# Kernel tuning notes

Hardware: AMD Instinct MI355X
Metric: run time of the kernel (lower is better)

The kernel has to match this reference:

```python
import jax, jax.numpy as jnp
import numpy as np

B, N, C = 32, 2048, 64  # graphs, points per graph, hidden channels


def _linear_params(key, fin, fout):
    k1, k2 = jax.random.split(key)
    bound = 1.0 / np.sqrt(fin)
    W = jax.random.uniform(k1, (fin, fout), minval=-bound, maxval=bound, dtype=jnp.float32)
    b = jax.random.uniform(k2, (fout,), minval=-bound, maxval=bound, dtype=jnp.float32)
    return W, b


def setup_inputs() -> dict:
    key = jax.random.key(0)
    ks = jax.random.split(key, 10)
    W1a, b1a = _linear_params(ks[0], 3 * 2 + 3, C)   # conv1 mlp layer 1 (h is pos, 3-dim)
    W1b, b1b = _linear_params(ks[1], C, C)
    W2a, b2a = _linear_params(ks[2], C * 2 + 3, C)   # conv2
    W2b, b2b = _linear_params(ks[3], C, C)
    W3a, b3a = _linear_params(ks[4], C * 2 + 3, C)   # conv3
    W3b, b3b = _linear_params(ks[5], C, C)
    Wr, br = _linear_params(ks[6], C, 6)
    pos = jax.random.normal(ks[7], (B * N, 3), dtype=jnp.float32)
    x = jax.random.normal(ks[8], (B * N, 3), dtype=jnp.float32)  # unused by forward (h=pos)
    batch = jnp.repeat(jnp.arange(B, dtype=jnp.int32), N)
    return dict(x=x, pos=pos, batch=batch,
                W1a=W1a, b1a=b1a, W1b=W1b, b1b=b1b,
                W2a=W2a, b2a=b2a, W2b=W2b, b2b=b2b,
                W3a=W3a, b3a=b3a, W3b=W3b, b3b=b3b,
                Wr=Wr, br=br)


_gather = jax.vmap(lambda a, i: a[i])  # per-graph fancy gather


def knn_idx(pos, k):
    # pos: [B, n, 3] -> idx [B, n, k] of k nearest neighbors (incl. self, loop=True)
    d2 = jnp.sum((pos[:, :, None, :] - pos[:, None, :, :]) ** 2, axis=-1)  # [B,n,n]
    _, idx = jax.lax.top_k(-d2, k)
    return idx


def fps_idx(pos_b, m):
    # farthest point sampling of m points from pos_b [n,3], deterministic start at 0
    d = jnp.sum((pos_b - pos_b[0]) ** 2, axis=-1)
    def body(d, _):
        i = jnp.argmax(d)
        d = jnp.minimum(d, jnp.sum((pos_b - pos_b[i]) ** 2, axis=-1))
        return d, i
    _, rest = jax.lax.scan(body, d, None, length=m - 1)
    return jnp.concatenate([jnp.zeros((1,), rest.dtype), rest])


def pointnet_layer(h, pos, idx, W1, b1, W2, b2):
    # h [B,n,Ch], pos [B,n,3], idx [B,n,k]; message = mlp(cat(h_i,h_j,pos_j-pos_i)); aggr = max
    h_j = _gather(h, idx)                      # [B,n,k,Ch]
    pos_j = _gather(pos, idx)                  # [B,n,k,3]
    rel = pos_j - pos[:, :, None, :]
    h_i = jnp.broadcast_to(h[:, :, None, :], h_j.shape)
    m = jnp.concatenate([h_i, h_j, rel], axis=-1)
    m = jax.nn.relu(m @ W1 + b1) @ W2 + b2
    return jnp.max(m, axis=2)                  # max over neighbors -> [B,n,C]


def reference(x, pos, batch,
              W1a, b1a, W1b, b1b,
              W2a, b2a, W2b, b2b,
              W3a, b3a, W3b, b3b,
              Wr, br):
    p = pos.reshape(B, N, 3)
    # layer 1: h = pos, k = 6
    h = jax.nn.relu(pointnet_layer(p, p, knn_idx(p, 6), W1a, b1a, W1b, b1b))
    # fps ratio 0.5 -> N/2
    sel = jax.vmap(lambda pb: fps_idx(pb, N // 2))(p)
    p, h = _gather(p, sel), _gather(h, sel)
    # layer 2: k = 4
    h = jax.nn.relu(pointnet_layer(h, p, knn_idx(p, 4), W2a, b2a, W2b, b2b))
    # fps -> N/4
    sel = jax.vmap(lambda pb: fps_idx(pb, N // 4))(p)
    p, h = _gather(p, sel), _gather(h, sel)
    # layer 3: k = 3
    h = jax.nn.relu(pointnet_layer(h, p, knn_idx(p, 3), W3a, b3a, W3b, b3b))
    g = jnp.max(h, axis=1)  # global max pool over points -> [B, C]
    return g @ Wr + br      # [B, 6]
```

## Files before the change

### kernel.cpp

```cpp
#include <hip/hip_runtime.h>
#include <hip/hip_bf16.h>
#include <math.h>

constexpr int B = 32;
constexpr int N = 2048;

__global__ void detect_kernel(const unsigned int* __restrict__ raw, int* __restrict__ flag) {
    __shared__ int cnt;
    if (threadIdx.x == 0) cnt = 0;
    __syncthreads();
    int c = 0;
    for (int i = threadIdx.x; i < 4096; i += 256) {
        unsigned h = (raw[i] >> 8) & 0x7f;
        if (h >= 0x3a && h <= 0x41) c++;
    }
    atomicAdd(&cnt, c);
    __syncthreads();
    if (threadIdx.x == 0) *flag = (cnt > (4096 * 55) / 100) ? 1 : 0;
}

__global__ void b2f_kernel(const void* __restrict__ in, float* __restrict__ out, int n,
                           const int* __restrict__ flag) {
    int i = blockIdx.x * 256 + threadIdx.x;
    if (i >= n) return;
    if (*flag) out[i] = __bfloat162float(((const __hip_bfloat16*)in)[i]);
    else       out[i] = ((const float*)in)[i];
}

struct B2FMulti {
    const void* src[14];
    float* dst[14];
    int n[14];
};

__global__ void b2f_multi_kernel(B2FMulti p, const int* __restrict__ flag) {
    int a = blockIdx.y;
    int i = blockIdx.x * 256 + threadIdx.x;
    if (i >= p.n[a]) return;
    if (*flag) p.dst[a][i] = __bfloat162float(((const __hip_bfloat16*)p.src[a])[i]);
    else       p.dst[a][i] = ((const float*)p.src[a])[i];
}

template <int K>
__global__ void __launch_bounds__(256) knn_kernel(const float* __restrict__ pos,
                                                  int* __restrict__ idx_out, int n) {
    #pragma clang fp contract(off)
    const int b = blockIdx.y;
    const int i = blockIdx.x * 256 + threadIdx.x;
    const float* pb = pos + (size_t)b * n * 3;
    const float xi = pb[i * 3 + 0], yi = pb[i * 3 + 1], zi = pb[i * 3 + 2];

    float bd[K];
    int   bi_[K];
    #pragma unroll
    for (int q = 0; q < K; ++q) { bd[q] = __builtin_inff(); bi_[q] = 0x7fffffff; }

    __shared__ float tx[256], ty[256], tz[256];
    for (int t0 = 0; t0 < n; t0 += 256) {
        __syncthreads();
        {
            int j = t0 + threadIdx.x;
            tx[threadIdx.x] = pb[j * 3 + 0];
            ty[threadIdx.x] = pb[j * 3 + 1];
            tz[threadIdx.x] = pb[j * 3 + 2];
        }
        __syncthreads();
        for (int jj = 0; jj < 256; ++jj) {
            float dx = xi - tx[jj], dy = yi - ty[jj], dz = zi - tz[jj];
            float d2 = (dx * dx + dy * dy) + dz * dz;
            int jg = t0 + jj;
            if (d2 < bd[K - 1] || (d2 == bd[K - 1] && jg < bi_[K - 1])) {
                bd[K - 1] = d2; bi_[K - 1] = jg;
                #pragma unroll
                for (int q = K - 1; q > 0; --q) {
                    bool sw = (bd[q] < bd[q - 1]) || (bd[q] == bd[q - 1] && bi_[q] < bi_[q - 1]);
                    if (sw) {
                        float td = bd[q]; bd[q] = bd[q - 1]; bd[q - 1] = td;
                        int   ti = bi_[q]; bi_[q] = bi_[q - 1]; bi_[q - 1] = ti;
                    }
                }
            }
        }
    }
    int* op = idx_out + ((size_t)b * n + i) * K;
    #pragma unroll
    for (int q = 0; q < K; ++q) op[q] = bi_[q];
}

template <int NPTS>
__device__ __forceinline__ void fps_phase(const float* __restrict__ px,
                                          const float* __restrict__ py,
                                          const float* __restrict__ pz,
                                          int* __restrict__ sel_lds,
                                          unsigned long long* __restrict__ slots,
                                          int m, int t) {
    #pragma clang fp contract(off)
    constexpr int P = NPTS / 256;
    float d[P], ox[P], oy[P], oz[P];
    unsigned int nk[P];
    const float sx = px[0], sy = py[0], sz = pz[0];
    #pragma unroll
    for (int p = 0; p < P; ++p) {
        const int ii = t * P + p;
        ox[p] = px[ii]; oy[p] = py[ii]; oz[p] = pz[ii];
        float dx = ox[p] - sx, dy = oy[p] - sy, dz = oz[p] - sz;
        d[p] = (dx * dx + dy * dy) + dz * dz;
        nk[p] = ~(unsigned)ii;
    }
    if (t == 0) sel_lds[0] = 0;

    for (int it = 1; it < m; ++it) {
        unsigned long long kb = ((unsigned long long)__float_as_uint(d[0]) << 32) | nk[0];
        #pragma unroll
        for (int p = 1; p < P; ++p) {
            unsigned long long key = ((unsigned long long)__float_as_uint(d[p]) << 32) | nk[p];
            if (key > kb) kb = key;
        }
        #pragma unroll
        for (int o = 1; o < 64; o <<= 1) {
            unsigned long long other = __shfl_xor(kb, o, 64);
            if (other > kb) kb = other;
        }
        if ((t & 63) == 0) slots[(it & 1) * 4 + (t >> 6)] = kb;
        __syncthreads();
        {
            const unsigned long long* sp = slots + (it & 1) * 4;
            unsigned long long k0 = sp[0], k1 = sp[1], k2 = sp[2], k3 = sp[3];
            if (k1 > k0) k0 = k1;
            if (k3 > k2) k2 = k3;
            kb = (k2 > k0) ? k2 : k0;
        }
        const int bix = (int)(~(unsigned)(kb & 0xffffffffULL));
        if (t == 0) sel_lds[it] = bix;
        const float nx = px[bix], ny = py[bix], nz = pz[bix];
        #pragma unroll
        for (int p = 0; p < P; ++p) {
            float dx = ox[p] - nx, dy = oy[p] - ny, dz = oz[p] - nz;
            float dd = (dx * dx + dy * dy) + dz * dz;
            d[p] = fminf(d[p], dd);
        }
    }
    __syncthreads();
}

__global__ void __launch_bounds__(256) mega_kernel(
        const float* __restrict__ posf, const int* __restrict__ idx1,
        const float* __restrict__ W1, const float* __restrict__ b1,
        const float* __restrict__ W2, const float* __restrict__ b2,
        float* __restrict__ h1, int* __restrict__ sel1, int* __restrict__ sel2,
        float* __restrict__ p2, float* __restrict__ p3) {
    __shared__ __align__(16) char smem[65536];
    const int t = threadIdx.x;

    if (blockIdx.x < B) {
        const int b = blockIdx.x;
        float* px = (float*)smem;
        float* py = px + 2048;
        float* pz = py + 2048;
        int*   sel1_l = (int*)(pz + 2048);
        float* qx = (float*)(sel1_l + 1024);
        float* qy = qx + 1024;
        float* qz = qy + 1024;
        int*   sel2_l = (int*)(qz + 1024);
        unsigned long long* slots = (unsigned long long*)(sel2_l + 512);

        const float* pb = posf + (size_t)b * N * 3;
        for (int i = t; i < N; i += 256) {
            px[i] = pb[i * 3 + 0]; py[i] = pb[i * 3 + 1]; pz[i] = pb[i * 3 + 2];
        }
        __syncthreads();

        fps_phase<2048>(px, py, pz, sel1_l, slots, 1024, t);

        for (int i = t; i < 1024; i += 256) {
            int s = sel1_l[i];
            qx[i] = px[s]; qy[i] = py[s]; qz[i] = pz[s];
            sel1[(size_t)b * 1024 + i] = s;
        }
        __syncthreads();
        for (int i = t; i < 1024; i += 256) {
            float* pp = p2 + ((size_t)b * 1024 + i) * 3;
            pp[0] = qx[i]; pp[1] = qy[i]; pp[2] = qz[i];
        }

        fps_phase<1024>(qx, qy, qz, sel2_l, slots, 512, t);

        for (int i = t; i < 512; i += 256) {
            int s = sel2_l[i];
            sel2[(size_t)b * 512 + i] = s;
            float* pp = p3 + ((size_t)b * 512 + i) * 3;
            pp[0] = qx[s]; pp[1] = qy[s]; pp[2] = qz[s];
        }
    } else {
        const int lane = t & 63, g = t >> 6;
        float* al = (float*)smem + g * 4096;
        const int flat = (blockIdx.x - B) * 256 + t;
        const int b = flat >> 11;
        const int i = flat & (N - 1);
        const float* pb = posf + (size_t)b * N * 3;
        const float xi = pb[i * 3 + 0], yi = pb[i * 3 + 1], zi = pb[i * 3 + 2];

        float acc[64];
        #pragma unroll
        for (int c = 0; c < 64; ++c) acc[c] = -__builtin_inff();

        const int* idxp = idx1 + (size_t)flat * 6;
        for (int kk = 0; kk < 6; ++kk) {
            const int j = idxp[kk];
            const float xj = pb[j * 3 + 0], yj = pb[j * 3 + 1], zj = pb[j * 3 + 2];
            const float mv[9] = {xi, yi, zi, xj, yj, zj, xj - xi, yj - yi, zj - zi};
            float a[64];
            #pragma unroll
            for (int e = 0; e < 64; ++e) a[e] = b1[e];
            #pragma unroll
            for (int d = 0; d < 9; ++d) {
                #pragma unroll
                for (int e = 0; e < 64; ++e) a[e] = fmaf(mv[d], W1[d * 64 + e], a[e]);
            }
            __syncthreads();
            #pragma unroll
            for (int e = 0; e < 64; ++e) al[e * 64 + lane] = fmaxf(a[e], 0.f);
            __syncthreads();
            float o[64];
            #pragma unroll
            for (int c = 0; c < 64; ++c) o[c] = b2[c];
            for (int e = 0; e < 64; ++e) {
                float av = al[e * 64 + lane];
                #pragma unroll
                for (int c = 0; c < 64; ++c) o[c] = fmaf(av, W2[e * 64 + c], o[c]);
            }
            #pragma unroll
            for (int c = 0; c < 64; ++c) acc[c] = fmaxf(acc[c], o[c]);
        }
        float* op = h1 + (size_t)flat * 64;
        #pragma unroll
        for (int c = 0; c < 64; ++c) op[c] = fmaxf(acc[c], 0.f);
    }
}

__global__ void gather_h_kernel(const float* __restrict__ h_in, const int* __restrict__ sel,
                                float* __restrict__ h_out, int n_in, int m) {
    const int b = blockIdx.y;
    const int tid = blockIdx.x * 256 + threadIdx.x;
    const int p = tid >> 6, c = tid & 63;
    if (p >= m) return;
    const int s = sel[(size_t)b * m + p];
    h_out[((size_t)b * m + p) * 64 + c] = h_in[((size_t)b * n_in + s) * 64 + c];
}

__global__ void __launch_bounds__(64) pointnet64_kernel(
        const float* __restrict__ h_in, const float* __restrict__ pos,
        const int* __restrict__ idx,
        const float* __restrict__ W1, const float* __restrict__ b1,
        const float* __restrict__ W2, const float* __restrict__ b2,
        float* __restrict__ out, int n, int k) {
    const int b = blockIdx.y, lane = threadIdx.x;
    const int i = blockIdx.x * 64 + lane;
    const float* pb = pos + (size_t)b * n * 3;
    const float* hb = h_in + (size_t)b * n * 64;
    const float xi = pb[i * 3 + 0], yi = pb[i * 3 + 1], zi = pb[i * 3 + 2];

    __shared__ float a_lds[64 * 64];

    float acc[64];
    #pragma unroll
    for (int c = 0; c < 64; ++c) acc[c] = -__builtin_inff();

    const int* idxp = idx + ((size_t)b * n + i) * k;
    const float* hi = hb + (size_t)i * 64;
    for (int kk = 0; kk < k; ++kk) {
        const int j = idxp[kk];
        const float xj = pb[j * 3 + 0], yj = pb[j * 3 + 1], zj = pb[j * 3 + 2];
        const float* hj = hb + (size_t)j * 64;

        float a[64];
        #pragma unroll
        for (int e = 0; e < 64; ++e) a[e] = b1[e];

        for (int d4 = 0; d4 < 16; ++d4) {
            float4 v = *(const float4*)(hi + d4 * 4);
            const float mu[4] = {v.x, v.y, v.z, v.w};
            const float* wr = W1 + (size_t)(d4 * 4) * 64;
            #pragma unroll
            for (int u = 0; u < 4; ++u) {
                #pragma unroll
                for (int e = 0; e < 64; ++e) a[e] = fmaf(mu[u], wr[u * 64 + e], a[e]);
            }
        }
        for (int d4 = 0; d4 < 16; ++d4) {
            float4 v = *(const float4*)(hj + d4 * 4);
            const float mu[4] = {v.x, v.y, v.z, v.w};
            const float* wr = W1 + (size_t)(64 + d4 * 4) * 64;
            #pragma unroll
            for (int u = 0; u < 4; ++u) {
                #pragma unroll
                for (int e = 0; e < 64; ++e) a[e] = fmaf(mu[u], wr[u * 64 + e], a[e]);
            }
        }
        {
            const float mr[3] = {xj - xi, yj - yi, zj - zi};
            #pragma unroll
            for (int d = 0; d < 3; ++d) {
                #pragma unroll
                for (int e = 0; e < 64; ++e) a[e] = fmaf(mr[d], W1[(128 + d) * 64 + e], a[e]);
            }
        }
        __syncthreads();
        #pragma unroll
        for (int e = 0; e < 64; ++e) a_lds[e * 64 + lane] = fmaxf(a[e], 0.f);
        __syncthreads();
        float o[64];
        #pragma unroll
        for (int c = 0; c < 64; ++c) o[c] = b2[c];
        for (int e = 0; e < 64; ++e) {
            float av = a_lds[e * 64 + lane];
            #pragma unroll
            for (int c = 0; c < 64; ++c) o[c] = fmaf(av, W2[e * 64 + c], o[c]);
        }
        #pragma unroll
        for (int c = 0; c < 64; ++c) acc[c] = fmaxf(acc[c], o[c]);
    }
    float* op = out + ((size_t)b * n + i) * 64;
    #pragma unroll
    for (int c = 0; c < 64; ++c) op[c] = fmaxf(acc[c], 0.f);
}

__global__ void __launch_bounds__(64) head_kernel(const float* __restrict__ h,
                                                  const float* __restrict__ Wr,
                                                  const float* __restrict__ br,
                                                  void* __restrict__ out, int n,
                                                  const int* __restrict__ flag) {
    const int b = blockIdx.x, lane = threadIdx.x;
    const float* hb = h + (size_t)b * n * 64;
    float g = -__builtin_inff();
    for (int i = 0; i < n; ++i) g = fmaxf(g, hb[(size_t)i * 64 + lane]);
    __shared__ float gl[64];
    gl[lane] = g;
    __syncthreads();
    if (lane < 6) {
        float o = br[lane];
        #pragma unroll
        for (int c = 0; c < 64; ++c) o = fmaf(gl[c], Wr[c * 6 + lane], o);
        if (*flag) ((__hip_bfloat16*)out)[b * 6 + lane] = __float2bfloat16(o);
        else       ((float*)out)[b * 6 + lane] = o;
    }
}

extern "C" void kernel_launch(void* const* d_in, const int* in_sizes, int n_in,
                              void* d_out, int out_size, void* d_ws, size_t ws_size,
                              hipStream_t stream) {
    (void)in_sizes; (void)n_in; (void)out_size; (void)ws_size;

    char* w = (char*)d_ws;
    auto alloc = [&](size_t nbytes) -> void* {
        void* p = (void*)w;
        w += (nbytes + 255) & ~(size_t)255;
        return p;
    };

    int*   flag = (int*)alloc(4);
    float* posf = (float*)alloc((size_t)B * N * 3 * 4);
    float* W1a = (float*)alloc(9 * 64 * 4);    float* b1a = (float*)alloc(64 * 4);
    float* W1b = (float*)alloc(64 * 64 * 4);   float* b1b = (float*)alloc(64 * 4);
    float* W2a = (float*)alloc(131 * 64 * 4);  float* b2a = (float*)alloc(64 * 4);
    float* W2b = (float*)alloc(64 * 64 * 4);   float* b2b = (float*)alloc(64 * 4);
    float* W3a = (float*)alloc(131 * 64 * 4);  float* b3a = (float*)alloc(64 * 4);
    float* W3b = (float*)alloc(64 * 64 * 4);   float* b3b = (float*)alloc(64 * 4);
    float* Wr  = (float*)alloc(64 * 6 * 4);    float* br  = (float*)alloc(6 * 4);

    float* h1    = (float*)alloc((size_t)B * N * 64 * 4);
    int*   idx1  = (int*)alloc((size_t)B * N * 6 * 4);
    int*   sel1  = (int*)alloc((size_t)B * 1024 * 4);
    float* p2    = (float*)alloc((size_t)B * 1024 * 3 * 4);
    float* h2in  = (float*)alloc((size_t)B * 1024 * 64 * 4);
    int*   idx2  = (int*)alloc((size_t)B * 1024 * 4 * 4);
    int*   sel2  = (int*)alloc((size_t)B * 512 * 4);
    float* p3    = (float*)alloc((size_t)B * 512 * 3 * 4);
    int*   idx3  = (int*)alloc((size_t)B * 512 * 3 * 4);
    float* h2out = h1;
    float* h3in  = h1 + (size_t)B * 1024 * 64;
    float* h3out = h1 + (size_t)B * 1024 * 64 + (size_t)B * 512 * 64;

    detect_kernel<<<dim3(1), 256, 0, stream>>>((const unsigned int*)d_in[1], flag);
    b2f_kernel<<<dim3((B * N * 3 + 255) / 256), 256, 0, stream>>>(d_in[1], posf, B * N * 3, flag);
    B2FMulti mp;
    {
        const int   wi[14] = {3, 4, 5, 6, 7, 8, 9, 10, 11, 12, 13, 14, 15, 16};
        float*      wd[14] = {W1a, b1a, W1b, b1b, W2a, b2a, W2b, b2b, W3a, b3a, W3b, b3b, Wr, br};
        const int   wn[14] = {576, 64, 4096, 64, 8384, 64, 4096, 64, 8384, 64, 4096, 64, 384, 6};
        for (int q = 0; q < 14; ++q) { mp.src[q] = d_in[wi[q]]; mp.dst[q] = wd[q]; mp.n[q] = wn[q]; }
    }
    b2f_multi_kernel<<<dim3(33, 14), 256, 0, stream>>>(mp, flag);

    knn_kernel<6><<<dim3(N / 256, B), 256, 0, stream>>>(posf, idx1, N);

    mega_kernel<<<dim3(B + (B * N) / 256), 256, 0, stream>>>(posf, idx1, W1a, b1a, W1b, b1b,
                                                             h1, sel1, sel2, p2, p3);

    gather_h_kernel<<<dim3(1024 * 64 / 256, B), 256, 0, stream>>>(h1, sel1, h2in, N, 1024);
    knn_kernel<4><<<dim3(1024 / 256, B), 256, 0, stream>>>(p2, idx2, 1024);
    pointnet64_kernel<<<dim3(1024 / 64, B), 64, 0, stream>>>(h2in, p2, idx2, W2a, b2a, W2b, b2b,
                                                             h2out, 1024, 4);

    gather_h_kernel<<<dim3(512 * 64 / 256, B), 256, 0, stream>>>(h2out, sel2, h3in, 1024, 512);
    knn_kernel<3><<<dim3(512 / 256, B), 256, 0, stream>>>(p3, idx3, 512);
    pointnet64_kernel<<<dim3(512 / 64, B), 64, 0, stream>>>(h3in, p3, idx3, W3a, b3a, W3b, b3b,
                                                            h3out, 512, 3);

    head_kernel<<<dim3(B), 64, 0, stream>>>(h3out, Wr, br, d_out, 512, flag);
}
```

Before: 2.276 ms.

## Split FPS from mega kernel, use DPP reductions, fuse gathers into pointnet

Result: faster. 2.090 ms (-8.2%).

```diff
diff --git a/kernel.cpp b/kernel.cpp
--- a/kernel.cpp
+++ b/kernel.cpp
@@ -19,26 +19,15 @@
     if (threadIdx.x == 0) *flag = (cnt > (4096 * 55) / 100) ? 1 : 0;
 }
 
-__global__ void b2f_kernel(const void* __restrict__ in, float* __restrict__ out, int n,
-                           const int* __restrict__ flag) {
+struct ConvSeg { const void* src; float* dst; int n; };
+struct ConvParams { ConvSeg s[15]; };
+
+__global__ void convert_kernel(ConvParams p, const int* __restrict__ flag) {
+    const ConvSeg sg = p.s[blockIdx.y];
     int i = blockIdx.x * 256 + threadIdx.x;
-    if (i >= n) return;
-    if (*flag) out[i] = __bfloat162float(((const __hip_bfloat16*)in)[i]);
-    else       out[i] = ((const float*)in)[i];
-}
-
-struct B2FMulti {
-    const void* src[14];
-    float* dst[14];
-    int n[14];
-};
-
-__global__ void b2f_multi_kernel(B2FMulti p, const int* __restrict__ flag) {
-    int a = blockIdx.y;
-    int i = blockIdx.x * 256 + threadIdx.x;
-    if (i >= p.n[a]) return;
-    if (*flag) p.dst[a][i] = __bfloat162float(((const __hip_bfloat16*)p.src[a])[i]);
-    else       p.dst[a][i] = ((const float*)p.src[a])[i];
+    if (i >= sg.n) return;
+    if (*flag) sg.dst[i] = __bfloat162float(((const __hip_bfloat16*)sg.src)[i]);
+    else       sg.dst[i] = ((const float*)sg.src)[i];
 }
 
 template <int K>
@@ -87,6 +76,10 @@
     for (int q = 0; q < K; ++q) op[q] = bi_[q];
 }
 
+#define DPP_MAXF(v, ctrl)                                                      \
+    (v) = fmaxf((v), __int_as_float(__builtin_amdgcn_update_dpp(               \
+        __float_as_int(v), __float_as_int(v), (ctrl), 0xf, 0xf, false)))
+
 template <int NPTS>
 __device__ __forceinline__ void fps_phase(const float* __restrict__ px,
                                           const float* __restrict__ py,
@@ -97,167 +90,97 @@
     #pragma clang fp contract(off)
     constexpr int P = NPTS / 256;
     float d[P], ox[P], oy[P], oz[P];
-    unsigned int nk[P];
-    const float sx = px[0], sy = py[0], sz = pz[0];
     #pragma unroll
     for (int p = 0; p < P; ++p) {
         const int ii = t * P + p;
         ox[p] = px[ii]; oy[p] = py[ii]; oz[p] = pz[ii];
-        float dx = ox[p] - sx, dy = oy[p] - sy, dz = oz[p] - sz;
-        d[p] = (dx * dx + dy * dy) + dz * dz;
-        nk[p] = ~(unsigned)ii;
+        d[p] = __builtin_inff();
     }
     if (t == 0) sel_lds[0] = 0;
+    float nx = px[0], ny = py[0], nz = pz[0];
 
     for (int it = 1; it < m; ++it) {
-        unsigned long long kb = ((unsigned long long)__float_as_uint(d[0]) << 32) | nk[0];
-        #pragma unroll
-        for (int p = 1; p < P; ++p) {
-            unsigned long long key = ((unsigned long long)__float_as_uint(d[p]) << 32) | nk[p];
-            if (key > kb) kb = key;
-        }
-        #pragma unroll
-        for (int o = 1; o < 64; o <<= 1) {
-            unsigned long long other = __shfl_xor(kb, o, 64);
-            if (other > kb) kb = other;
-        }
-        if ((t & 63) == 0) slots[(it & 1) * 4 + (t >> 6)] = kb;
-        __syncthreads();
-        {
-            const unsigned long long* sp = slots + (it & 1) * 4;
-            unsigned long long k0 = sp[0], k1 = sp[1], k2 = sp[2], k3 = sp[3];
-            if (k1 > k0) k0 = k1;
-            if (k3 > k2) k2 = k3;
-            kb = (k2 > k0) ? k2 : k0;
-        }
-        const int bix = (int)(~(unsigned)(kb & 0xffffffffULL));
-        if (t == 0) sel_lds[it] = bix;
-        const float nx = px[bix], ny = py[bix], nz = pz[bix];
+        float bv = -1.0f; int bix = 0;
         #pragma unroll
         for (int p = 0; p < P; ++p) {
             float dx = ox[p] - nx, dy = oy[p] - ny, dz = oz[p] - nz;
             float dd = (dx * dx + dy * dy) + dz * dz;
-            d[p] = fminf(d[p], dd);
-        }
-    }
-    __syncthreads();
-}
-
-__global__ void __launch_bounds__(256) mega_kernel(
-        const float* __restrict__ posf, const int* __restrict__ idx1,
-        const float* __restrict__ W1, const float* __restrict__ b1,
-        const float* __restrict__ W2, const float* __restrict__ b2,
-        float* __restrict__ h1, int* __restrict__ sel1, int* __restrict__ sel2,
+            float dn = fminf(d[p], dd);
+            d[p] = dn;
+            if (dn > bv) { bv = dn; bix = t * P + p; }
+        }
+        float r = bv;
+        DPP_MAXF(r, 0x111); DPP_MAXF(r, 0x112); DPP_MAXF(r, 0x114);
+        DPP_MAXF(r, 0x118); DPP_MAXF(r, 0x142); DPP_MAXF(r, 0x143);
+        const float gmax = __int_as_float(__builtin_amdgcn_readlane(__float_as_int(r), 63));
+        const unsigned long long msk = __ballot(bv == gmax);
+        const int wl = (int)__builtin_ctzll(msk);
+        const int widx = __builtin_amdgcn_readlane(bix, wl);
+        if ((t & 63) == 0) {
+            slots[(it & 1) * 4 + (t >> 6)] =
+                ((unsigned long long)(unsigned)__float_as_int(gmax) << 32) |
+                (unsigned)(~widx);
+        }
+        __syncthreads();
+        const unsigned long long* sp = slots + (it & 1) * 4;
+        unsigned long long k0 = sp[0], k1 = sp[1], k2 = sp[2], k3 = sp[3];
+        if (k1 > k0) k0 = k1;
+        if (k3 > k2) k2 = k3;
+        if (k2 > k0) k0 = k2;
+        const int g = ~(int)(unsigned)(k0 & 0xffffffffULL);
+        if (t == 0) sel_lds[it] = g;
+        nx = px[g]; ny = py[g]; nz = pz[g];
+    }
+    __syncthreads();
+}
+
+__global__ void __launch_bounds__(256) fps_only_kernel(
+        const float* __restrict__ posf, int* __restrict__ sel1, int* __restrict__ sel2,
         float* __restrict__ p2, float* __restrict__ p3) {
-    __shared__ __align__(16) char smem[65536];
+    __shared__ float px[2048], py[2048], pz[2048];
+    __shared__ float qx[1024], qy[1024], qz[1024];
+    __shared__ int sel1_l[1024], sel2_l[512];
+    __shared__ unsigned long long slots[8];
     const int t = threadIdx.x;
-
-    if (blockIdx.x < B) {
-        const int b = blockIdx.x;
-        float* px = (float*)smem;
-        float* py = px + 2048;
-        float* pz = py + 2048;
-        int*   sel1_l = (int*)(pz + 2048);
-        float* qx = (float*)(sel1_l + 1024);
-        float* qy = qx + 1024;
-        float* qz = qy + 1024;
-        int*   sel2_l = (int*)(qz + 1024);
-        unsigned long long* slots = (unsigned long long*)(sel2_l + 512);
-
-        const float* pb = posf + (size_t)b * N * 3;
-        for (int i = t; i < N; i += 256) {
-            px[i] = pb[i * 3 + 0]; py[i] = pb[i * 3 + 1]; pz[i] = pb[i * 3 + 2];
-        }
-        __syncthreads();
-
-        fps_phase<2048>(px, py, pz, sel1_l, slots, 1024, t);
-
-        for (int i = t; i < 1024; i += 256) {
-            int s = sel1_l[i];
-            qx[i] = px[s]; qy[i] = py[s]; qz[i] = pz[s];
-            sel1[(size_t)b * 1024 + i] = s;
-        }
-        __syncthreads();
-        for (int i = t; i < 1024; i += 256) {
-            float* pp = p2 + ((size_t)b * 1024 + i) * 3;
-            pp[0] = qx[i]; pp[1] = qy[i]; pp[2] = qz[i];
-        }
-
-        fps_phase<1024>(qx, qy, qz, sel2_l, slots, 512, t);
-
-        for (int i = t; i < 512; i += 256) {
-            int s = sel2_l[i];
-            sel2[(size_t)b * 512 + i] = s;
-            float* pp = p3 + ((size_t)b * 512 + i) * 3;
-            pp[0] = qx[s]; pp[1] = qy[s]; pp[2] = qz[s];
-        }
-    } else {
-        const int lane = t & 63, g = t >> 6;
-        float* al = (float*)smem + g * 4096;
-        const int flat = (blockIdx.x - B) * 256 + t;
-        const int b = flat >> 11;
-        const int i = flat & (N - 1);
-        const float* pb = posf + (size_t)b * N * 3;
-        const float xi = pb[i * 3 + 0], yi = pb[i * 3 + 1], zi = pb[i * 3 + 2];
-
-        float acc[64];
-        #pragma unroll
-        for (int c = 0; c < 64; ++c) acc[c] = -__builtin_inff();
-
-        const int* idxp = idx1 + (size_t)flat * 6;
-        for (int kk = 0; kk < 6; ++kk) {
-            const int j = idxp[kk];
-            const float xj = pb[j * 3 + 0], yj = pb[j * 3 + 1], zj = pb[j * 3 + 2];
-            const float mv[9] = {xi, yi, zi, xj, yj, zj, xj - xi, yj - yi, zj - zi};
-            float a[64];
-            #pragma unroll
-            for (int e = 0; e < 64; ++e) a[e] = b1[e];
-            #pragma unroll
-            for (int d = 0; d < 9; ++d) {
-                #pragma unroll
-                for (int e = 0; e < 64; ++e) a[e] = fmaf(mv[d], W1[d * 64 + e], a[e]);
-            }
-            __syncthreads();
-            #pragma unroll
-            for (int e = 0; e < 64; ++e) al[e * 64 + lane] = fmaxf(a[e], 0.f);
-            __syncthreads();
-            float o[64];
-            #pragma unroll
-            for (int c = 0; c < 64; ++c) o[c] = b2[c];
-            for (int e = 0; e < 64; ++e) {
-                float av = al[e * 64 + lane];
-                #pragma unroll
-                for (int c = 0; c < 64; ++c) o[c] = fmaf(av, W2[e * 64 + c], o[c]);
-            }
-            #pragma unroll
-            for (int c = 0; c < 64; ++c) acc[c] = fmaxf(acc[c], o[c]);
-        }
-        float* op = h1 + (size_t)flat * 64;
-        #pragma unroll
-        for (int c = 0; c < 64; ++c) op[c] = fmaxf(acc[c], 0.f);
-    }
-}
-
-__global__ void gather_h_kernel(const float* __restrict__ h_in, const int* __restrict__ sel,
-                                float* __restrict__ h_out, int n_in, int m) {
-    const int b = blockIdx.y;
-    const int tid = blockIdx.x * 256 + threadIdx.x;
-    const int p = tid >> 6, c = tid & 63;
-    if (p >= m) return;
-    const int s = sel[(size_t)b * m + p];
-    h_out[((size_t)b * m + p) * 64 + c] = h_in[((size_t)b * n_in + s) * 64 + c];
-}
-
-__global__ void __launch_bounds__(64) pointnet64_kernel(
-        const float* __restrict__ h_in, const float* __restrict__ pos,
-        const int* __restrict__ idx,
+    const int b = blockIdx.x;
+
+    const float* pb = posf + (size_t)b * N * 3;
+    for (int i = t; i < N; i += 256) {
+        px[i] = pb[i * 3 + 0]; py[i] = pb[i * 3 + 1]; pz[i] = pb[i * 3 + 2];
+    }
+    __syncthreads();
+
+    fps_phase<2048>(px, py, pz, sel1_l, slots, 1024, t);
+
+    for (int i = t; i < 1024; i += 256) {
+        int s = sel1_l[i];
+        qx[i] = px[s]; qy[i] = py[s]; qz[i] = pz[s];
+        sel1[(size_t)b * 1024 + i] = s;
+    }
+    __syncthreads();
+    for (int i = t; i < 1024; i += 256) {
+        float* pp = p2 + ((size_t)b * 1024 + i) * 3;
+        pp[0] = qx[i]; pp[1] = qy[i]; pp[2] = qz[i];
+    }
+
+    fps_phase<1024>(qx, qy, qz, sel2_l, slots, 512, t);
+
+    for (int i = t; i < 512; i += 256) {
+        int s = sel2_l[i];
+        sel2[(size_t)b * 512 + i] = s;
+        float* pp = p3 + ((size_t)b * 512 + i) * 3;
+        pp[0] = qx[s]; pp[1] = qy[s]; pp[2] = qz[s];
+    }
+}
+
+__global__ void __launch_bounds__(64) pointnet3_kernel(
+        const float* __restrict__ pos, const int* __restrict__ idx,
         const float* __restrict__ W1, const float* __restrict__ b1,
         const float* __restrict__ W2, const float* __restrict__ b2,
         float* __restrict__ out, int n, int k) {
     const int b = blockIdx.y, lane = threadIdx.x;
     const int i = blockIdx.x * 64 + lane;
     const float* pb = pos + (size_t)b * n * 3;
-    const float* hb = h_in + (size_t)b * n * 64;
     const float xi = pb[i * 3 + 0], yi = pb[i * 3 + 1], zi = pb[i * 3 + 2];
 
     __shared__ float a_lds[64 * 64];
@@ -267,11 +190,63 @@
     for (int c = 0; c < 64; ++c) acc[c] = -__builtin_inff();
 
     const int* idxp = idx + ((size_t)b * n + i) * k;
-    const float* hi = hb + (size_t)i * 64;
     for (int kk = 0; kk < k; ++kk) {
         const int j = idxp[kk];
         const float xj = pb[j * 3 + 0], yj = pb[j * 3 + 1], zj = pb[j * 3 + 2];
-        const float* hj = hb + (size_t)j * 64;
+        const float mv[9] = {xi, yi, zi, xj, yj, zj, xj - xi, yj - yi, zj - zi};
+        float a[64];
+        #pragma unroll
+        for (int e = 0; e < 64; ++e) a[e] = b1[e];
+        #pragma unroll
+        for (int d = 0; d < 9; ++d) {
+            #pragma unroll
+            for (int e = 0; e < 64; ++e) a[e] = fmaf(mv[d], W1[d * 64 + e], a[e]);
+        }
+        __syncthreads();
+        #pragma unroll
+        for (int e = 0; e < 64; ++e) a_lds[e * 64 + lane] = fmaxf(a[e], 0.f);
+        __syncthreads();
+        float o[64];
+        #pragma unroll
+        for (int c = 0; c < 64; ++c) o[c] = b2[c];
+        for (int e = 0; e < 64; ++e) {
+            float av = a_lds[e * 64 + lane];
+            #pragma unroll
+            for (int c = 0; c < 64; ++c) o[c] = fmaf(av, W2[e * 64 + c], o[c]);
+        }
+        #pragma unroll
+        for (int c = 0; c < 64; ++c) acc[c] = fmaxf(acc[c], o[c]);
+    }
+    float* op = out + ((size_t)b * n + i) * 64;
+    #pragma unroll
+    for (int c = 0; c < 64; ++c) op[c] = fmaxf(acc[c], 0.f);
+}
+
+__global__ void __launch_bounds__(64) pointnet64_kernel(
+        const float* __restrict__ h_base, const float* __restrict__ pos,
+        const int* __restrict__ sel, const int* __restrict__ idx,
+        const float* __restrict__ W1, const float* __restrict__ b1,
+        const float* __restrict__ W2, const float* __restrict__ b2,
+        float* __restrict__ out, int n_base, int n, int k) {
+    const int b = blockIdx.y, lane = threadIdx.x;
+    const int i = blockIdx.x * 64 + lane;
+    const float* pb = pos + (size_t)b * n * 3;
+    const float* hb = h_base + (size_t)b * n_base * 64;
+    const int* selb = sel + (size_t)b * n;
+    const float xi = pb[i * 3 + 0], yi = pb[i * 3 + 1], zi = pb[i * 3 + 2];
+
+    __shared__ float a_lds[64 * 64];
+
+    float acc[64];
+    #pragma unroll
+    for (int c = 0; c < 64; ++c) acc[c] = -__builtin_inff();
+
+    const int* idxp = idx + ((size_t)b * n + i) * k;
+    const float* hi = hb + (size_t)selb[i] * 64;
+    for (int kk = 0; kk < k; ++kk) {
+        const int j = idxp[kk];
+        const float xj = pb[j * 3 + 0], yj = pb[j * 3 + 1], zj = pb[j * 3 + 2];
+        const float* hj = hb + (size_t)selb[j] * 64;
 
         float a[64];
         #pragma unroll
@@ -368,44 +343,39 @@
     float* W3b = (float*)alloc(64 * 64 * 4);   float* b3b = (float*)alloc(64 * 4);
     float* Wr  = (float*)alloc(64 * 6 * 4);    float* br  = (float*)alloc(6 * 4);
 
-    float* h1    = (float*)alloc((size_t)B * N * 64 * 4);
-    int*   idx1  = (int*)alloc((size_t)B * N * 6 * 4);
-    int*   sel1  = (int*)alloc((size_t)B * 1024 * 4);
-    float* p2    = (float*)alloc((size_t)B * 1024 * 3 * 4);
-    float* h2in  = (float*)alloc((size_t)B * 1024 * 64 * 4);
-    int*   idx2  = (int*)alloc((size_t)B * 1024 * 4 * 4);
-    int*   sel2  = (int*)alloc((size_t)B * 512 * 4);
-    float* p3    = (float*)alloc((size_t)B * 512 * 3 * 4);
-    int*   idx3  = (int*)alloc((size_t)B * 512 * 3 * 4);
-    float* h2out = h1;
-    float* h3in  = h1 + (size_t)B * 1024 * 64;
-    float* h3out = h1 + (size_t)B * 1024 * 64 + (size_t)B * 512 * 64;
+    float* h1   = (float*)alloc((size_t)B * N * 64 * 4);
+    float* h2   = (float*)alloc((size_t)B * 1024 * 64 * 4);
+    float* h3   = (float*)alloc((size_t)B * 512 * 64 * 4);
+    int*   idx1 = (int*)alloc((size_t)B * N * 6 * 4);
+    int*   idx2 = (int*)alloc((size_t)B * 1024 * 4 * 4);
+    int*   idx3 = (int*)alloc((size_t)B * 512 * 3 * 4);
+    int*   sel1 = (int*)alloc((size_t)B * 1024 * 4);
+    int*   sel2 = (int*)alloc((size_t)B * 512 * 4);
+    float* p2   = (float*)alloc((size_t)B * 1024 * 3 * 4);
+    float* p3   = (float*)alloc((size_t)B * 512 * 3 * 4);
 
     detect_kernel<<<dim3(1), 256, 0, stream>>>((const unsigned int*)d_in[1], flag);
-    b2f_kernel<<<dim3((B * N * 3 + 255) / 256), 256, 0, stream>>>(d_in[1], posf, B * N * 3, flag);
-    B2FMulti mp;
+    ConvParams cp;
     {
-        const int   wi[14] = {3, 4, 5, 6, 7, 8, 9, 10, 11, 12, 13, 14, 15, 16};
-        float*      wd[14] = {W1a, b1a, W1b, b1b, W2a, b2a, W2b, b2b, W3a, b3a, W3b, b3b, Wr, br};
-        const int   wn[14] = {576, 64, 4096, 64, 8384, 64, 4096, 64, 8384, 64, 4096, 64, 384, 6};
-        for (int q = 0; q < 14; ++q) { mp.src[q] = d_in[wi[q]]; mp.dst[q] = wd[q]; mp.n[q] = wn[q]; }
-    }
-    b2f_multi_kernel<<<dim3(33, 14), 256, 0, stream>>>(mp, flag);
+        float* wd[15] = {posf, W1a, b1a, W1b, b1b, W2a, b2a, W2b, b2b, W3a, b3a, W3b, b3b, Wr, br};
+        const int wi[15] = {1, 3, 4, 5, 6, 7, 8, 9, 10, 11, 12, 13, 14, 15, 16};
+        const int wn[15] = {B * N * 3, 576, 64, 4096, 64, 8384, 64, 4096, 64, 8384, 64, 4096, 64, 384, 6};
+        for (int q = 0; q < 15; ++q) { cp.s[q].src = d_in[wi[q]]; cp.s[q].dst = wd[q]; cp.s[q].n = wn[q]; }
+    }
+    convert_kernel<<<dim3((B * N * 3 + 255) / 256, 15), 256, 0, stream>>>(cp, flag);
+
+    fps_only_kernel<<<dim3(B), 256, 0, stream>>>(posf, sel1, sel2, p2, p3);
 
     knn_kernel<6><<<dim3(N / 256, B), 256, 0, stream>>>(posf, idx1, N);
-
-    mega_kernel<<<dim3(B + (B * N) / 256), 256, 0, stream>>>(posf, idx1, W1a, b1a, W1b, b1b,
-                                                             h1, sel1, sel2, p2, p3);
-
-    gather_h_kernel<<<dim3(1024 * 64 / 256, B), 256, 0, stream>>>(h1, sel1, h2in, N, 1024);
+    pointnet3_kernel<<<dim3(N / 64, B), 64, 0, stream>>>(posf, idx1, W1a, b1a, W1b, b1b, h1, N, 6);
+
     knn_kernel<4><<<dim3(1024 / 256, B), 256, 0, stream>>>(p2, idx2, 1024);
-    pointnet64_kernel<<<dim3(1024 / 64, B), 64, 0, stream>>>(h2in, p2, idx2, W2a, b2a, W2b, b2b,
-                                                             h2out, 1024, 4);
-
-    gather_h_kernel<<<dim3(512 * 64 / 256, B), 256, 0, stream>>>(h2out, sel2, h3in, 1024, 512);
+    pointnet64_kernel<<<dim3(1024 / 64, B), 64, 0, stream>>>(h1, p2, sel1, idx2,
+                                                             W2a, b2a, W2b, b2b, h2, N, 1024, 4);
+
     knn_kernel<3><<<dim3(512 / 256, B), 256, 0, stream>>>(p3, idx3, 512);
-    pointnet64_kernel<<<dim3(512 / 64, B), 64, 0, stream>>>(h3in, p3, idx3, W3a, b3a, W3b, b3b,
-                                                            h3out, 512, 3);
-
-    head_kernel<<<dim3(B), 64, 0, stream>>>(h3out, Wr, br, d_out, 512, flag);
-}
+    pointnet64_kernel<<<dim3(512 / 64, B), 64, 0, stream>>>(h2, p3, sel2, idx3,
+                                                            W3a, b3a, W3b, b3b, h3, 1024, 512, 3);
+
+    head_kernel<<<dim3(B), 64, 0, stream>>>(h3, Wr, br, d_out, 512, flag);
+}
```
